# Kernel optimization log

Measured on AMD Instinct MI355X. Metric: run time of the kernel, lower is better.

The kernel has to match this reference:

```python
import jax, jax.numpy as jnp
import numpy as np
from jax import lax

B, L, D, F, K = 16, 1024, 384, 1536, 3
MAX_DUR = 10          # clamp on per-token duration (makes output length static)
T_OUT = L * MAX_DUR   # padded expanded length
ALPHA = 1.0
EPS = 1e-5


def conv1d_same(x_ncl, w, b):
    # x_ncl: [B, Cin, L], w: [Cout, Cin, K]
    y = lax.conv_general_dilated(x_ncl, w, window_strides=(1,), padding='SAME',
                                 dimension_numbers=('NCH', 'OIH', 'NCH'))
    return y + b[None, :, None]


def conv_block(x, wA, bA, wB, bB):
    # x: [B, L, D] -> Conv(D->F) ReLU Conv(F->D) ReLU -> [B, L, D]
    h = x.transpose(0, 2, 1)
    h = jax.nn.relu(conv1d_same(h, wA, bA))
    h = jax.nn.relu(conv1d_same(h, wB, bB))
    return h.transpose(0, 2, 1)


def layernorm(x, g, b):
    mu = jnp.mean(x, axis=-1, keepdims=True)
    var = jnp.var(x, axis=-1, keepdims=True)
    return (x - mu) * lax.rsqrt(var + EPS) * g + b


def setup_inputs() -> dict:
    key = jax.random.key(0)
    ks = jax.random.split(key, 8)
    s = 0.02
    return {
        'y': jax.random.normal(ks[0], (B, L, D), jnp.float32),
        'token_lengths': jax.random.randint(ks[1], (B,), 1, L + 1).astype(jnp.int32),
        'w1a': jax.random.normal(ks[2], (F, D, K), jnp.float32) * s,
        'b1a': jnp.zeros((F,), jnp.float32),
        'w1b': jax.random.normal(ks[3], (D, F, K), jnp.float32) * s,
        'b1b': jnp.zeros((D,), jnp.float32),
        'g1': jnp.ones((D,), jnp.float32),
        'be1': jnp.zeros((D,), jnp.float32),
        'w2a': jax.random.normal(ks[4], (F, D, K), jnp.float32) * s,
        'b2a': jnp.zeros((F,), jnp.float32),
        'w2b': jax.random.normal(ks[5], (D, F, K), jnp.float32) * s,
        'b2b': jnp.zeros((D,), jnp.float32),
        'g2': jnp.ones((D,), jnp.float32),
        'be2': jnp.zeros((D,), jnp.float32),
        'wl': jax.random.normal(ks[6], (D, 1), jnp.float32) * s,
        'bl': jnp.zeros((1,), jnp.float32),
    }


def reference(y, token_lengths, w1a, b1a, w1b, b1b, g1, be1,
              w2a, b2a, w2b, b2b, g2, be2, wl, bl):
    # DurationPredictor (eval mode: dropout is identity)
    h = conv_block(y, w1a, b1a, w1b, b1b)
    h = layernorm(h, g1, be1)
    h = conv_block(h, w2a, b2a, w2b, b2b)
    h = layernorm(h, g2, be2)
    preds = h @ wl + bl                      # [B, L, 1]

    # lengths = round(alpha * exp(preds)), masked to valid tokens, clamped
    lns = jnp.round(ALPHA * jnp.exp(preds[..., 0]))
    lns = jnp.clip(lns, 0, MAX_DUR).astype(jnp.int32)        # [B, L]
    mask = jnp.arange(L)[None, :] < token_lengths[:, None]
    lns = jnp.where(mask, lns, 0)

    # ragged repeat_interleave + pad, fully vectorized:
    # output frame t maps to token idx = searchsorted(cumsum(lns), t, 'right')
    csum = jnp.cumsum(lns, axis=1)                            # [B, L]
    totals = csum[:, -1]                                      # [B]
    t = jnp.arange(T_OUT, dtype=jnp.int32)
    idx = jax.vmap(lambda c: jnp.searchsorted(c, t, side='right'))(csum)  # [B, T_OUT]
    idx = jnp.minimum(idx, L - 1)
    gathered = jnp.take_along_axis(y, idx[..., None], axis=1)  # [B, T_OUT, D]
    valid = t[None, :] < totals[:, None]
    enlarged = jnp.where(valid[..., None], gathered, 0.0)
    return enlarged, totals
```

## Files before the change

### kernel.cpp

```cpp
#include <hip/hip_runtime.h>
#include <hip/hip_bf16.h>

#define BB 16
#define LL 1024
#define DD 384
#define FF 1536
#define KK 3
#define T_OUT 10240
#define MAX_DUR 10

#define PADL 1026
#define LO_SCALE 2048.0f
#define LO_INV   4.8828125e-4f

typedef _Float16 f16x8 __attribute__((ext_vector_type(8)));
typedef float    f32x4 __attribute__((ext_vector_type(4)));

__device__ __forceinline__ void gll16(const void* g, void* l) {
    __builtin_amdgcn_global_load_lds(
        (const __attribute__((address_space(1))) void*)g,
        (__attribute__((address_space(3))) void*)l, 16, 0, 0);
}

__device__ __forceinline__ void split_write(float v, _Float16* hi, _Float16* lo, size_t off) {
    _Float16 h = (_Float16)v;
    hi[off] = h;
    lo[off] = (_Float16)((v - (float)h) * LO_SCALE);
}

__device__ __forceinline__ float split_read(const _Float16* hi, const _Float16* lo, size_t off) {
    return (float)hi[off] + (float)lo[off] * LO_INV;
}

__global__ void wfrag_k(const float* __restrict__ w, _Float16* __restrict__ hi,
                        _Float16* __restrict__ lo, int O, int I) {
    int id = blockIdx.x * 256 + threadIdx.x;
    int total = O * 3 * I;
    if (id >= total) return;
    int e = id & 7;
    int lane = (id >> 3) & 63;
    int rest = id >> 9;
    int nKT = (3 * I) >> 5;
    int ktl = rest % nKT;
    int ot = rest / nKT;
    int o = ot * 16 + (lane & 15);
    int koff = ((lane >> 4) << 3) + e;
    int kseg = ktl % 3;
    int i = (ktl / 3) * 32 + koff;
    float v = w[(o * I + i) * 3 + kseg];
    split_write(v, hi, lo, id);
}

__global__ void ysplit_k(const float* __restrict__ y, _Float16* __restrict__ hi,
                         _Float16* __restrict__ lo) {
    int id = blockIdx.x * 256 + threadIdx.x;
    if (id >= BB * PADL * DD) return;
    int d = id % DD;
    int r = id / DD;
    int b = r / PADL;
    int lr = r - b * PADL;
    float v = 0.f;
    if (lr >= 1 && lr <= LL) v = y[((size_t)(b << 10) + (lr - 1)) * DD + d];
    split_write(v, hi, lo, id);
}

__global__ void padzero_k(_Float16* __restrict__ hi, _Float16* __restrict__ lo, int width) {
    int id = blockIdx.x * 256 + threadIdx.x;
    if (id >= BB * 2 * width) return;
    int b = id / (2 * width);
    int rem = id - b * 2 * width;
    int row = (rem / width) ? (PADL - 1) : 0;
    int c = rem % width;
    size_t off = (size_t)(b * PADL + row) * width + c;
    hi[off] = (_Float16)0.f;
    lo[off] = (_Float16)0.f;
}

template<int MI>
__global__ __launch_bounds__(256, 2) void gemm_split(
        const _Float16* __restrict__ Ahi, const _Float16* __restrict__ Alo,
        const _Float16* __restrict__ WfH, const _Float16* __restrict__ WfL,
        const float* __restrict__ bias,
        _Float16* __restrict__ Ohi, _Float16* __restrict__ Olo,
        int Cin, int Cout, int Ktot, int nN) {
    constexpr int BM   = MI * 32;
    constexpr int BUFH = MI * 1024;
    constexpr int NIT  = MI / 2;
    constexpr int VMK  = 8 + 4 * NIT;
    __shared__ _Float16 lds_h[8 * BUFH];
    const int tid = threadIdx.x;
    const int lane = tid & 63;
    const int w = tid >> 6;
    const int lm = lane & 15, lq = lane >> 4;
    const int xcd = blockIdx.x & 7;
    const int t2 = blockIdx.x >> 3;
    const int g  = t2 / (4 * nN);
    const int r  = t2 - g * (4 * nN);
    const int n_t = r >> 2;
    const int mi  = r & 3;
    const int m_t = ((g * 4 + mi) << 3) + xcd;
    const int m0 = m_t * BM;
    const int n0 = n_t << 7;
    const int b = m0 >> 10;
    const int l0 = m0 & 1023;
    const int rowBase = b * PADL + l0;
    const int wm = (w >> 1) * (MI * 16), wn = (w & 1) * 64;

    f32x4 accM[MI][4], accC[MI][4];
    const f32x4 zz = {0.f, 0.f, 0.f, 0.f};
    #pragma unroll
    for (int i = 0; i < MI; ++i)
        #pragma unroll
        for (int jj = 0; jj < 4; ++jj) { accM[i][jj] = zz; accC[i][jj] = zz; }

    const int nKT = Ktot >> 5;

    auto stageA = [&](int kt, int bidx) {
        int kseg = kt % 3;
        int d0 = (kt / 3) << 5;
        #pragma unroll
        for (int it = 0; it < NIT; ++it) {
            int s = (w * NIT + it) * 64 + lane;
            int p = s >> 3, sl = s & 7;
            int t = sl ^ (p & 7);
            int m = p * 2 + (t >> 2);
            int k8 = t & 3;
            size_t aoff = (size_t)(rowBase + m + kseg) * Cin + d0 + k8 * 8;
            _Float16* lbase = lds_h + (size_t)bidx * (2 * BUFH) + (size_t)(w * NIT + it) * 512;
            gll16(Ahi + aoff, lbase);
            gll16(Alo + aoff, lbase + BUFH);
        }
    };

    auto loadB = [&](int kt, f16x8* bH, f16x8* bL) {
        int ktc = kt < nKT ? kt : nKT - 1;
        #pragma unroll
        for (int jj = 0; jj < 4; ++jj) {
            int ntg = (n0 + wn + jj * 16) >> 4;
            size_t boff = (((size_t)ntg * nKT + ktc) * 64 + lane) * 8;
            bH[jj] = *(const f16x8*)(WfH + boff);
            bL[jj] = *(const f16x8*)(WfL + boff);
        }
    };

    auto compute = [&](const _Float16* lb, const f16x8* bH, const f16x8* bL) {
        __builtin_amdgcn_s_setprio(1);
        #pragma unroll
        for (int i = 0; i < MI; ++i) {
            int m = wm + i * 16 + lm;
            int p = m >> 1;
            int sl = (((m & 1) << 2) | lq) ^ (p & 7);
            int off = p * 64 + sl * 8;
            f16x8 aH = *(const f16x8*)(lb + off);
            f16x8 aL = *(const f16x8*)(lb + BUFH + off);
            #pragma unroll
            for (int jj = 0; jj < 4; ++jj) {
                accM[i][jj] = __builtin_amdgcn_mfma_f32_16x16x32_f16(aH, bH[jj], accM[i][jj], 0, 0, 0);
                accC[i][jj] = __builtin_amdgcn_mfma_f32_16x16x32_f16(aH, bL[jj], accC[i][jj], 0, 0, 0);
                accC[i][jj] = __builtin_amdgcn_mfma_f32_16x16x32_f16(aL, bH[jj], accC[i][jj], 0, 0, 0);
            }
        }
        __builtin_amdgcn_s_setprio(0);
    };

    f16x8 b0H[4], b0L[4], b1H[4], b1L[4];
    stageA(0, 0);
    loadB(0, b0H, b0L);
    stageA(1, 1);
    for (int kt = 0; kt < nKT; kt += 2) {
        loadB(kt + 1, b1H, b1L);
        stageA(kt + 2 < nKT ? kt + 2 : nKT - 1, (kt + 2) & 3);
        __builtin_amdgcn_sched_barrier(0);
        asm volatile("s_waitcnt vmcnt(%0)" :: "i"(VMK) : "memory");
        __builtin_amdgcn_s_barrier();
        __builtin_amdgcn_sched_barrier(0);
        compute(lds_h + (size_t)(kt & 3) * (2 * BUFH), b0H, b0L);
        loadB(kt + 2, b0H, b0L);
        stageA(kt + 3 < nKT ? kt + 3 : nKT - 1, (kt + 3) & 3);
        __builtin_amdgcn_sched_barrier(0);
        asm volatile("s_waitcnt vmcnt(%0)" :: "i"(VMK) : "memory");
        __builtin_amdgcn_s_barrier();
        __builtin_amdgcn_sched_barrier(0);
        compute(lds_h + (size_t)((kt + 1) & 3) * (2 * BUFH), b1H, b1L);
    }
    #pragma unroll
    for (int i = 0; i < MI; ++i)
        #pragma unroll
        for (int jj = 0; jj < 4; ++jj) {
            int n_g = n0 + wn + jj * 16 + lm;
            float bv = bias[n_g];
            #pragma unroll
            for (int rr = 0; rr < 4; ++rr) {
                int l = l0 + wm + i * 16 + lq * 4 + rr;
                float v = accM[i][jj][rr] + accC[i][jj][rr] * LO_INV + bv;
                v = fmaxf(v, 0.f);
                size_t off = (size_t)(b * PADL + 1 + l) * Cout + n_g;
                split_write(v, Ohi, Olo, off);
            }
        }
}

__global__ __launch_bounds__(128) void ln_split_k(
        _Float16* __restrict__ hi, _Float16* __restrict__ lo,
        const float* __restrict__ g, const float* __restrict__ be) {
    const int row = blockIdx.x;
    const int b = row >> 10, l = row & 1023;
    const size_t base = (size_t)(b * PADL + 1 + l) * DD;
    const int tid = threadIdx.x;
    float v0 = split_read(hi, lo, base + tid);
    float v1 = split_read(hi, lo, base + tid + 128);
    float v2 = split_read(hi, lo, base + tid + 256);

    __shared__ float sh[2];
    float s = v0 + v1 + v2;
    #pragma unroll
    for (int o = 32; o > 0; o >>= 1) s += __shfl_down(s, o, 64);
    if ((tid & 63) == 0) sh[tid >> 6] = s;
    __syncthreads();
    float mu = (sh[0] + sh[1]) * (1.f / DD);
    __syncthreads();
    float d0 = v0 - mu, d1 = v1 - mu, d2 = v2 - mu;
    float q = d0 * d0 + d1 * d1 + d2 * d2;
    #pragma unroll
    for (int o = 32; o > 0; o >>= 1) q += __shfl_down(q, o, 64);
    if ((tid & 63) == 0) sh[tid >> 6] = q;
    __syncthreads();
    float var = (sh[0] + sh[1]) * (1.f / DD);
    float rs = rsqrtf(var + 1e-5f);
    split_write(d0 * rs * g[tid] + be[tid], hi, lo, base + tid);
    split_write(d1 * rs * g[tid + 128] + be[tid + 128], hi, lo, base + tid + 128);
    split_write(d2 * rs * g[tid + 256] + be[tid + 256], hi, lo, base + tid + 256);
}

__global__ __launch_bounds__(128) void ln_pred_split_k(
        const _Float16* __restrict__ hi, const _Float16* __restrict__ lo,
        const float* __restrict__ g, const float* __restrict__ be,
        const float* __restrict__ wl, const float* __restrict__ bl,
        const int* __restrict__ token_lengths, int* __restrict__ lns) {
    const int row = blockIdx.x;
    const int b = row >> 10, l = row & 1023;
    const size_t base = (size_t)(b * PADL + 1 + l) * DD;
    const int tid = threadIdx.x;
    float v0 = split_read(hi, lo, base + tid);
    float v1 = split_read(hi, lo, base + tid + 128);
    float v2 = split_read(hi, lo, base + tid + 256);

    __shared__ float sh[2];
    float s = v0 + v1 + v2;
    #pragma unroll
    for (int o = 32; o > 0; o >>= 1) s += __shfl_down(s, o, 64);
    if ((tid & 63) == 0) sh[tid >> 6] = s;
    __syncthreads();
    float mu = (sh[0] + sh[1]) * (1.f / DD);
    __syncthreads();
    float d0 = v0 - mu, d1 = v1 - mu, d2 = v2 - mu;
    float q = d0 * d0 + d1 * d1 + d2 * d2;
    #pragma unroll
    for (int o = 32; o > 0; o >>= 1) q += __shfl_down(q, o, 64);
    if ((tid & 63) == 0) sh[tid >> 6] = q;
    __syncthreads();
    float var = (sh[0] + sh[1]) * (1.f / DD);
    float rs = rsqrtf(var + 1e-5f);
    __syncthreads();
    float p = (d0 * rs * g[tid]       + be[tid])       * wl[tid]
            + (d1 * rs * g[tid + 128] + be[tid + 128]) * wl[tid + 128]
            + (d2 * rs * g[tid + 256] + be[tid + 256]) * wl[tid + 256];
    #pragma unroll
    for (int o = 32; o > 0; o >>= 1) p += __shfl_down(p, o, 64);
    if ((tid & 63) == 0) sh[tid >> 6] = p;
    __syncthreads();
    if (tid == 0) {
        float pred = sh[0] + sh[1] + bl[0];
        float e = expf(pred);
        float r = rintf(e);
        r = fminf(fmaxf(r, 0.f), (float)MAX_DUR);
        int v = (int)r;
        if (l >= token_lengths[b]) v = 0;
        lns[row] = v;
    }
}

__global__ __launch_bounds__(1024) void cumsum_k(
        const int* __restrict__ lns, int* __restrict__ csum,
        float* __restrict__ totals_out) {
    __shared__ int s[1024];
    const int b = blockIdx.x, tid = threadIdx.x;
    s[tid] = lns[(b << 10) + tid];
    __syncthreads();
    #pragma unroll
    for (int o = 1; o < 1024; o <<= 1) {
        int t = (tid >= o) ? s[tid - o] : 0;
        __syncthreads();
        s[tid] += t;
        __syncthreads();
    }
    csum[(b << 10) + tid] = s[tid];
    if (tid == 1023) totals_out[b] = (float)s[1023];
}

__global__ __launch_bounds__(256) void gather_k(
        const float* __restrict__ y, const int* __restrict__ csum,
        float* __restrict__ out) {
    int gid = blockIdx.x * 256 + threadIdx.x;
    int c4 = gid % 96;
    int rest = gid / 96;
    int t = rest % T_OUT;
    int b = rest / T_OUT;
    const int* c = csum + (b << 10);
    int total = c[1023];
    float4 r = make_float4(0.f, 0.f, 0.f, 0.f);
    if (t < total) {
        int lo = 0, hi = 1024;
        while (lo < hi) {
            int mid = (lo + hi) >> 1;
            if (c[mid] <= t) lo = mid + 1; else hi = mid;
        }
        int idx = min(lo, LL - 1);
        r = *(const float4*)(y + ((size_t)((b << 10) + idx)) * DD + (c4 << 2));
    }
    *(float4*)(out + ((size_t)b * T_OUT + t) * DD + (c4 << 2)) = r;
}

extern "C" void kernel_launch(void* const* d_in, const int* in_sizes, int n_in,
                              void* d_out, int out_size, void* d_ws, size_t ws_size,
                              hipStream_t stream) {
    const float* y   = (const float*)d_in[0];
    const int*   tok = (const int*)d_in[1];
    const float* w1a = (const float*)d_in[2];
    const float* b1a = (const float*)d_in[3];
    const float* w1b = (const float*)d_in[4];
    const float* b1b = (const float*)d_in[5];
    const float* g1  = (const float*)d_in[6];
    const float* be1 = (const float*)d_in[7];
    const float* w2a = (const float*)d_in[8];
    const float* b2a = (const float*)d_in[9];
    const float* w2b = (const float*)d_in[10];
    const float* b2b = (const float*)d_in[11];
    const float* g2  = (const float*)d_in[12];
    const float* be2 = (const float*)d_in[13];
    const float* wl  = (const float*)d_in[14];
    const float* bl  = (const float*)d_in[15];

    float* out = (float*)d_out;

    const size_t WN   = (size_t)FF * DD * KK;
    const size_t SN   = (size_t)BB * PADL * DD;
    const size_t H1N  = (size_t)BB * PADL * FF;
    _Float16* p = (_Float16*)d_ws;
    _Float16* Wh1a = p;              _Float16* Wl1a = Wh1a + WN;
    _Float16* Wh1b = Wl1a + WN;      _Float16* Wl1b = Wh1b + WN;
    _Float16* Wh2a = Wl1b + WN;      _Float16* Wl2a = Wh2a + WN;
    _Float16* Wh2b = Wl2a + WN;      _Float16* Wl2b = Wh2b + WN;
    _Float16* Shi  = Wl2b + WN;      _Float16* Slo  = Shi + SN;
    _Float16* H1hi = Slo + SN;       _Float16* H1lo = H1hi + H1N;
    int* lns  = (int*)(H1lo + H1N);
    int* csum = lns + BB * LL;

    const int M = BB * LL;

    {
        int n = FF * DD * KK;
        wfrag_k<<<(n + 255) / 256, 256, 0, stream>>>(w1a, Wh1a, Wl1a, FF, DD);
        wfrag_k<<<(n + 255) / 256, 256, 0, stream>>>(w1b, Wh1b, Wl1b, DD, FF);
        wfrag_k<<<(n + 255) / 256, 256, 0, stream>>>(w2a, Wh2a, Wl2a, FF, DD);
        wfrag_k<<<(n + 255) / 256, 256, 0, stream>>>(w2b, Wh2b, Wl2b, DD, FF);
        int ny = BB * PADL * DD;
        ysplit_k<<<(ny + 255) / 256, 256, 0, stream>>>(y, Shi, Slo);
        int np = BB * 2 * FF;
        padzero_k<<<(np + 255) / 256, 256, 0, stream>>>(H1hi, H1lo, FF);
    }
    gemm_split<4><<<(FF / 128) * (M / 128), 256, 0, stream>>>(Shi, Slo, Wh1a, Wl1a, b1a, H1hi, H1lo, DD, FF, 3 * DD, FF / 128);
    gemm_split<2><<<(DD / 128) * (M / 64), 256, 0, stream>>>(H1hi, H1lo, Wh1b, Wl1b, b1b, Shi, Slo, FF, DD, 3 * FF, DD / 128);
    ln_split_k<<<M, 128, 0, stream>>>(Shi, Slo, g1, be1);
    gemm_split<4><<<(FF / 128) * (M / 128), 256, 0, stream>>>(Shi, Slo, Wh2a, Wl2a, b2a, H1hi, H1lo, DD, FF, 3 * DD, FF / 128);
    gemm_split<2><<<(DD / 128) * (M / 64), 256, 0, stream>>>(H1hi, H1lo, Wh2b, Wl2b, b2b, Shi, Slo, FF, DD, 3 * FF, DD / 128);
    ln_pred_split_k<<<M, 128, 0, stream>>>(Shi, Slo, g2, be2, wl, bl, tok, lns);
    cumsum_k<<<BB, 1024, 0, stream>>>(lns, csum, out + (size_t)BB * T_OUT * DD);
    {
        long long n = (long long)BB * T_OUT * 96;
        gather_k<<<(int)((n + 255) / 256), 256, 0, stream>>>(y, csum, out);
    }
}
```

Measured before the change: 1.038 ms.

## Reuse one A tile across the three conv taps and stage B through LDS

The conv-as-GEMM kernel now loads a single A tile of BM+2 rows per 32-channel slice and reads it three times with a row shift for each kernel tap. Before, it reloaded a separate shifted A tile for every tap. B weight fragments now go through double-buffered LDS with async global-to-LDS loads rather than per-wave register loads, and the pipeline is rebuilt around the three-tap inner structure with extra barriers. Occupancy is made a template parameter, raised to 3 for the F->D GEMM. The aim is to cut global A traffic roughly threefold; the cost is more barriers per iteration and possible LDS bank conflicts or register pressure.

Result: faster. 950.7 us (-8.4%).

```diff
diff --git a/kernel.cpp b/kernel.cpp
--- a/kernel.cpp
+++ b/kernel.cpp
@@ -76,18 +76,23 @@
     lo[off] = (_Float16)0.f;
 }
 
-template<int MI>
-__global__ __launch_bounds__(256, 2) void gemm_split(
+template<int MI, int OCC>
+__global__ __launch_bounds__(256, OCC) void gemm_split(
         const _Float16* __restrict__ Ahi, const _Float16* __restrict__ Alo,
         const _Float16* __restrict__ WfH, const _Float16* __restrict__ WfL,
         const float* __restrict__ bias,
         _Float16* __restrict__ Ohi, _Float16* __restrict__ Olo,
         int Cin, int Cout, int Ktot, int nN) {
     constexpr int BM   = MI * 32;
-    constexpr int BUFH = MI * 1024;
-    constexpr int NIT  = MI / 2;
-    constexpr int VMK  = 8 + 4 * NIT;
-    __shared__ _Float16 lds_h[8 * BUFH];
+    constexpr int AC   = (BM + 2) * 4;
+    constexpr int AC4  = AC / 4;
+    constexpr int AIT  = (AC4 + 63) / 64;
+    constexpr int NA   = 2 * AIT;
+    constexpr int AHH  = AC * 8;
+    constexpr int ABH  = 4 * AHH;
+    constexpr int KEEP0  = 4;
+    constexpr int KEEP12 = NA + 4;
+    __shared__ __align__(16) _Float16 lds_h[ABH + 2 * 8192];
     const int tid = threadIdx.x;
     const int lane = tid & 63;
     const int w = tid >> 6;
@@ -114,45 +119,57 @@
         for (int jj = 0; jj < 4; ++jj) { accM[i][jj] = zz; accC[i][jj] = zz; }
 
     const int nKT = Ktot >> 5;
-
-    auto stageA = [&](int kt, int bidx) {
-        int kseg = kt % 3;
-        int d0 = (kt / 3) << 5;
-        #pragma unroll
-        for (int it = 0; it < NIT; ++it) {
-            int s = (w * NIT + it) * 64 + lane;
+    const int nJ  = nKT / 3;
+
+    auto stageA = [&](int jt, int bidx) {
+        int d0 = jt << 5;
+        _Float16* abase = lds_h + bidx * (2 * AHH);
+        #pragma unroll
+        for (int it = 0; it < AIT; ++it) {
+            int cl = it * 64 + lane;
+            int s  = w * AC4 + cl;
             int p = s >> 3, sl = s & 7;
             int t = sl ^ (p & 7);
             int m = p * 2 + (t >> 2);
             int k8 = t & 3;
-            size_t aoff = (size_t)(rowBase + m + kseg) * Cin + d0 + k8 * 8;
-            _Float16* lbase = lds_h + (size_t)bidx * (2 * BUFH) + (size_t)(w * NIT + it) * 512;
-            gll16(Ahi + aoff, lbase);
-            gll16(Alo + aoff, lbase + BUFH);
+            size_t aoff = (size_t)(rowBase + m) * Cin + d0 + k8 * 8;
+            _Float16* hb = abase + (size_t)(w * AC4 + it * 64) * 8;
+            if (cl < AC4) {
+                gll16(Ahi + aoff, hb);
+                gll16(Alo + aoff, hb + AHH);
+            }
         }
     };
 
-    auto loadB = [&](int kt, f16x8* bH, f16x8* bL) {
+    auto stageB = [&](int kt, int bidx) {
         int ktc = kt < nKT ? kt : nKT - 1;
+        _Float16* bb = lds_h + ABH + bidx * 8192 + (w * 2) * 512;
+        #pragma unroll
+        for (int q = 0; q < 2; ++q) {
+            int ntg = (n0 >> 4) + w * 2 + q;
+            size_t boff = (((size_t)ntg * nKT + ktc) * 64 + lane) * 8;
+            gll16(WfH + boff, bb + q * 512);
+            gll16(WfL + boff, bb + 4096 + q * 512);
+        }
+    };
+
+    auto compute = [&](const _Float16* ab, const _Float16* bb, int kseg) {
+        f16x8 bH[4], bL[4];
         #pragma unroll
         for (int jj = 0; jj < 4; ++jj) {
-            int ntg = (n0 + wn + jj * 16) >> 4;
-            size_t boff = (((size_t)ntg * nKT + ktc) * 64 + lane) * 8;
-            bH[jj] = *(const f16x8*)(WfH + boff);
-            bL[jj] = *(const f16x8*)(WfL + boff);
-        }
-    };
-
-    auto compute = [&](const _Float16* lb, const f16x8* bH, const f16x8* bL) {
+            int nl = (w & 1) * 4 + jj;
+            bH[jj] = *(const f16x8*)(bb + nl * 512 + lane * 8);
+            bL[jj] = *(const f16x8*)(bb + 4096 + nl * 512 + lane * 8);
+        }
         __builtin_amdgcn_s_setprio(1);
         #pragma unroll
         for (int i = 0; i < MI; ++i) {
-            int m = wm + i * 16 + lm;
-            int p = m >> 1;
-            int sl = (((m & 1) << 2) | lq) ^ (p & 7);
+            int row = wm + i * 16 + lm + kseg;
+            int p = row >> 1;
+            int sl = (((row & 1) << 2) | lq) ^ (p & 7);
             int off = p * 64 + sl * 8;
-            f16x8 aH = *(const f16x8*)(lb + off);
-            f16x8 aL = *(const f16x8*)(lb + BUFH + off);
+            f16x8 aH = *(const f16x8*)(ab + off);
+            f16x8 aL = *(const f16x8*)(ab + AHH + off);
             #pragma unroll
             for (int jj = 0; jj < 4; ++jj) {
                 accM[i][jj] = __builtin_amdgcn_mfma_f32_16x16x32_f16(aH, bH[jj], accM[i][jj], 0, 0, 0);
@@ -163,25 +180,42 @@
         __builtin_amdgcn_s_setprio(0);
     };
 
-    f16x8 b0H[4], b0L[4], b1H[4], b1L[4];
+    stageB(0, 0);
+    __builtin_amdgcn_sched_barrier(0);
     stageA(0, 0);
-    loadB(0, b0H, b0L);
-    stageA(1, 1);
-    for (int kt = 0; kt < nKT; kt += 2) {
-        loadB(kt + 1, b1H, b1L);
-        stageA(kt + 2 < nKT ? kt + 2 : nKT - 1, (kt + 2) & 3);
-        __builtin_amdgcn_sched_barrier(0);
-        asm volatile("s_waitcnt vmcnt(%0)" :: "i"(VMK) : "memory");
-        __builtin_amdgcn_s_barrier();
-        __builtin_amdgcn_sched_barrier(0);
-        compute(lds_h + (size_t)(kt & 3) * (2 * BUFH), b0H, b0L);
-        loadB(kt + 2, b0H, b0L);
-        stageA(kt + 3 < nKT ? kt + 3 : nKT - 1, (kt + 3) & 3);
-        __builtin_amdgcn_sched_barrier(0);
-        asm volatile("s_waitcnt vmcnt(%0)" :: "i"(VMK) : "memory");
-        __builtin_amdgcn_s_barrier();
-        __builtin_amdgcn_sched_barrier(0);
-        compute(lds_h + (size_t)((kt + 1) & 3) * (2 * BUFH), b1H, b1L);
+    __builtin_amdgcn_sched_barrier(0);
+    stageB(1, 1);
+    __builtin_amdgcn_sched_barrier(0);
+
+    for (int j = 0; j < nJ; ++j) {
+        const _Float16* ab = lds_h + (j & 1) * (2 * AHH);
+        const int kt = 3 * j;
+        asm volatile("s_waitcnt vmcnt(%0)" :: "i"(KEEP0) : "memory");
+        __builtin_amdgcn_s_barrier();
+        __builtin_amdgcn_sched_barrier(0);
+        compute(ab, lds_h + ABH + (kt & 1) * 8192, 0);
+        __builtin_amdgcn_sched_barrier(0);
+        __builtin_amdgcn_s_barrier();
+        stageB(kt + 2, kt & 1);
+        __builtin_amdgcn_sched_barrier(0);
+        stageA(j + 1 < nJ ? j + 1 : j, (j + 1) & 1);
+        __builtin_amdgcn_sched_barrier(0);
+        asm volatile("s_waitcnt vmcnt(%0)" :: "i"(KEEP12) : "memory");
+        __builtin_amdgcn_s_barrier();
+        __builtin_amdgcn_sched_barrier(0);
+        compute(ab, lds_h + ABH + ((kt + 1) & 1) * 8192, 1);
+        __builtin_amdgcn_sched_barrier(0);
+        __builtin_amdgcn_s_barrier();
+        stageB(kt + 3, (kt + 1) & 1);
+        __builtin_amdgcn_sched_barrier(0);
+        asm volatile("s_waitcnt vmcnt(%0)" :: "i"(KEEP12) : "memory");
+        __builtin_amdgcn_s_barrier();
+        __builtin_amdgcn_sched_barrier(0);
+        compute(ab, lds_h + ABH + (kt & 1) * 8192, 2);
+        __builtin_amdgcn_sched_barrier(0);
+        __builtin_amdgcn_s_barrier();
+        stageB(kt + 4, kt & 1);
+        __builtin_amdgcn_sched_barrier(0);
     }
     #pragma unroll
     for (int i = 0; i < MI; ++i)
@@ -369,11 +403,11 @@
         int np = BB * 2 * FF;
         padzero_k<<<(np + 255) / 256, 256, 0, stream>>>(H1hi, H1lo, FF);
     }
-    gemm_split<4><<<(FF / 128) * (M / 128), 256, 0, stream>>>(Shi, Slo, Wh1a, Wl1a, b1a, H1hi, H1lo, DD, FF, 3 * DD, FF / 128);
-    gemm_split<2><<<(DD / 128) * (M / 64), 256, 0, stream>>>(H1hi, H1lo, Wh1b, Wl1b, b1b, Shi, Slo, FF, DD, 3 * FF, DD / 128);
+    gemm_split<4, 2><<<(FF / 128) * (M / 128), 256, 0, stream>>>(Shi, Slo, Wh1a, Wl1a, b1a, H1hi, H1lo, DD, FF, 3 * DD, FF / 128);
+    gemm_split<2, 3><<<(DD / 128) * (M / 64), 256, 0, stream>>>(H1hi, H1lo, Wh1b, Wl1b, b1b, Shi, Slo, FF, DD, 3 * FF, DD / 128);
     ln_split_k<<<M, 128, 0, stream>>>(Shi, Slo, g1, be1);
-    gemm_split<4><<<(FF / 128) * (M / 128), 256, 0, stream>>>(Shi, Slo, Wh2a, Wl2a, b2a, H1hi, H1lo, DD, FF, 3 * DD, FF / 128);
-    gemm_split<2><<<(DD / 128) * (M / 64), 256, 0, stream>>>(H1hi, H1lo, Wh2b, Wl2b, b2b, Shi, Slo, FF, DD, 3 * FF, DD / 128);
+    gemm_split<4, 2><<<(FF / 128) * (M / 128), 256, 0, stream>>>(Shi, Slo, Wh2a, Wl2a, b2a, H1hi, H1lo, DD, FF, 3 * DD, FF / 128);
+    gemm_split<2, 3><<<(DD / 128) * (M / 64), 256, 0, stream>>>(H1hi, H1lo, Wh2b, Wl2b, b2b, Shi, Slo, FF, DD, 3 * FF, DD / 128);
     ln_pred_split_k<<<M, 128, 0, stream>>>(Shi, Slo, g2, be2, wl, bl, tok, lns);
     cumsum_k<<<BB, 1024, 0, stream>>>(lns, csum, out + (size_t)BB * T_OUT * DD);
     {
```
